# Kernel optimization log

Measured on AMD Instinct MI355X. Metric: run time of the kernel, lower is better.

Reference implementation:

```python
import jax, jax.numpy as jnp
import numpy as np
import math

NFEAT = 1024
NHID = 512
NLAYERS = 8
LAMDA = 0.5
ALPHA = 0.1
N_DIA = 48
DIA_L = 64
N = N_DIA * DIA_L


def setup_inputs() -> dict:
    key = jax.random.key(0)
    ks = jax.random.split(key, 16)
    stdv_fc = 1.0 / math.sqrt(NFEAT)
    stdv_gc = 1.0 / math.sqrt(NHID)
    inp = {
        'a': jax.random.normal(ks[0], (N, NFEAT), jnp.float32),
        'v': jax.random.normal(ks[1], (N, NFEAT), jnp.float32),
        'l': jax.random.normal(ks[2], (N, NFEAT), jnp.float32),
        'W0': jax.random.uniform(ks[3], (NFEAT, NHID), jnp.float32, -stdv_fc, stdv_fc),
        'b0': jax.random.uniform(ks[4], (NHID,), jnp.float32, -stdv_fc, stdv_fc),
        'W1': jax.random.uniform(ks[5], (NFEAT, NHID), jnp.float32, -stdv_fc, stdv_fc),
        'b1': jax.random.uniform(ks[6], (NHID,), jnp.float32, -stdv_fc, stdv_fc),
        'W2': jax.random.uniform(ks[7], (NFEAT, NHID), jnp.float32, -stdv_fc, stdv_fc),
        'b2': jax.random.uniform(ks[8], (NHID,), jnp.float32, -stdv_fc, stdv_fc),
        'Wconv': jax.random.uniform(ks[9], (NLAYERS, NHID, NHID), jnp.float32, -stdv_gc, stdv_gc),
        'dia_len': DIA_L,  # uniform dialogue length
        'topicLabel': jnp.zeros((N,), jnp.int64),
    }
    return inp


def create_big_adj(a, v, l, dia_l):
    n = a.shape[0]
    d = n // dia_l
    feats = jnp.stack([a, v, l])                    # [3, N, F]
    x = feats.reshape(3, d, dia_l, -1)              # [3, D, L, F]
    nrm = x / jnp.sqrt(jnp.sum(x * x, axis=-1, keepdims=True))
    cos = jnp.einsum('mdif,mdjf->mdij', nrm, nrm) * 0.99999
    sim = jnp.arccos(cos)                           # [3, D, L, L]
    adj = jnp.zeros((3 * n, 3 * n), dtype=a.dtype)
    base = jnp.arange(d)[:, None, None] * dia_l     # dialogue start offsets
    rows = jnp.broadcast_to(base + jnp.arange(dia_l)[:, None], (d, dia_l, dia_l))
    cols = jnp.broadcast_to(base + jnp.arange(dia_l)[None, :], (d, dia_l, dia_l))
    for m in range(3):  # same-modality block-diagonal acos-similarity blocks
        adj = adj.at[m * n + rows, m * n + cols].set(sim[m])
    k = jnp.arange(n)
    for m in range(3):  # cross-modal: same-utterance links set to 0.99999
        for mm in range(3):
            if m != mm:
                adj = adj.at[m * n + k, mm * n + k].set(0.99999)
    dsum = jnp.sum(adj, axis=1)
    dinv = dsum ** -0.5
    return dinv[:, None] * adj * dinv[None, :]


def reference(a, v, l, W0, b0, W1, b1, W2, b2, Wconv, dia_len, topicLabel):
    relu = jax.nn.relu
    # eval mode: dropout is identity
    a_ = relu(a @ W0 + b0)
    l_ = relu(l @ W1 + b1)
    v_ = relu(v @ W2 + b2)
    x = jnp.concatenate([a_, v_, l_], axis=0)       # [3N, nhidden]
    adj = create_big_adj(a, v, l, dia_len)
    h0 = x
    h = x
    for i in range(NLAYERS):
        theta = math.log(LAMDA / (i + 1) + 1.0)
        hi = adj @ h
        support = (1.0 - ALPHA) * hi + ALPHA * h0
        h = relu(theta * (support @ Wconv[i]) + (1.0 - theta) * support)
    n = a.shape[0]
    out = jnp.concatenate([h[:n], h[n:2 * n], h[2 * n:]], axis=-1)  # [N, 3*nhidden]
    out = jnp.concatenate([l, out], axis=-1)        # use_residue
    return out
```

## Files before the change

### kernel.cpp

```cpp
#include <hip/hip_runtime.h>
#include <hip/hip_bf16.h>
#include <cmath>

#define NFEAT 1024
#define NHID  512
#define NLAYERS 8
#define NDIA 48
#define DIAL 64
#define NROW (NDIA*DIAL)
#define NROW3 (3*NROW)

typedef short bf16x8 __attribute__((ext_vector_type(8)));
typedef float f32x4  __attribute__((ext_vector_type(4)));
typedef unsigned short u16x8 __attribute__((ext_vector_type(8)));
typedef unsigned short u16x4 __attribute__((ext_vector_type(4)));
typedef unsigned short ushort_t;

__device__ __forceinline__ unsigned short f2bf(float x) {
  __hip_bfloat16 h = __float2bfloat16(x);
  return __builtin_bit_cast(unsigned short, h);
}
__device__ __forceinline__ float bf2f(unsigned short u) {
  __hip_bfloat16 h = __builtin_bit_cast(__hip_bfloat16, u);
  return __bfloat162float(h);
}

__device__ __forceinline__ void gload16(const void* g, void* l) {
  __builtin_amdgcn_global_load_lds(
      (const __attribute__((address_space(1))) void*)g,
      (__attribute__((address_space(3))) void*)l, 16, 0, 0);
}

__global__ __launch_bounds__(256) void k_prep(const float* __restrict__ a, const float* __restrict__ v,
                      const float* __restrict__ l, ushort_t* __restrict__ Abuf,
                      ushort_t* __restrict__ Xn) {
  int gid = blockIdx.x * 256 + threadIdx.x;
  int row = gid >> 6, lane = gid & 63;
  int m = row / NROW, r = row % NROW;
  const float* src = (m == 0 ? a : (m == 1 ? v : l)) + (size_t)r * NFEAT;
  float4 x[4];
  float s = 0.f;
#pragma unroll
  for (int q = 0; q < 4; ++q) {
    x[q] = *reinterpret_cast<const float4*>(src + lane * 4 + q * 256);
    s += x[q].x*x[q].x + x[q].y*x[q].y + x[q].z*x[q].z + x[q].w*x[q].w;
  }
#pragma unroll
  for (int off = 32; off; off >>= 1) s += __shfl_xor(s, off);
  float inv = rsqrtf(s);
  ushort_t* da = Abuf + (size_t)row * NFEAT;
  ushort_t* dn = Xn + (size_t)row * NFEAT;
#pragma unroll
  for (int q = 0; q < 4; ++q) {
    u16x4 oa, on;
    oa[0] = f2bf(x[q].x); oa[1] = f2bf(x[q].y); oa[2] = f2bf(x[q].z); oa[3] = f2bf(x[q].w);
    on[0] = f2bf(x[q].x * inv); on[1] = f2bf(x[q].y * inv);
    on[2] = f2bf(x[q].z * inv); on[3] = f2bf(x[q].w * inv);
    *reinterpret_cast<u16x4*>(da + lane * 4 + q * 256) = oa;
    *reinterpret_cast<u16x4*>(dn + lane * 4 + q * 256) = on;
  }
}

__global__ __launch_bounds__(256) void k_simm(const ushort_t* __restrict__ Xn,
                      ushort_t* __restrict__ Sbf, float* __restrict__ dinv) {
  __shared__ short Xs[2][4096];
  __shared__ float simS[64][73];
  int blk = blockIdx.x;
  const ushort_t* Xb = Xn + (size_t)blk * 64 * NFEAT;
  int t = threadIdx.x, w = t >> 6, lane = t & 63;
  f32x4 acc[4] = {};

#define STAGE_SIM(b, k0) do { \
    _Pragma("unroll") \
    for (int q = 0; q < 2; ++q) { \
      int f_ = t * 8 + q * 2048; \
      int row_ = f_ >> 6; \
      int col_ = (f_ & 63) ^ ((row_ & 7) << 3); \
      gload16(Xb + (size_t)row_ * NFEAT + (k0) + col_, (void*)(Xs[b] + q * 2048 + w * 512)); \
    } } while (0)

  STAGE_SIM(0, 0);
  __syncthreads();
  for (int it = 0; it < 16; ++it) {
    int cur = it & 1;
    if (it < 15) STAGE_SIM(cur ^ 1, (it + 1) * 64);
    const char* base = (const char*)Xs[cur];
#pragma unroll
    for (int ks = 0; ks < 2; ++ks) {
      int koff = ks * 32 + (lane >> 4) * 8;
      int arow = w * 16 + (lane & 15);
      bf16x8 af = *(const bf16x8*)(base + (((arow << 7) + (koff << 1)) ^ ((arow & 7) << 4)));
#pragma unroll
      for (int j = 0; j < 4; ++j) {
        int brow = j * 16 + (lane & 15);
        bf16x8 bf = *(const bf16x8*)(base + (((brow << 7) + (koff << 1)) ^ ((brow & 7) << 4)));
        acc[j] = __builtin_amdgcn_mfma_f32_16x16x32_bf16(af, bf, acc[j], 0, 0, 0);
      }
    }
    __syncthreads();
  }
#undef STAGE_SIM

#pragma unroll
  for (int j = 0; j < 4; ++j)
#pragma unroll
    for (int e = 0; e < 4; ++e) {
      int r = w * 16 + (lane >> 4) * 4 + e;
      int c = j * 16 + (lane & 15);
      float cc = acc[j][e] * 0.99999f;
      cc = fminf(fmaxf(cc, -0.99999f), 0.99999f);
      simS[r][c] = acosf(cc);
    }
  __syncthreads();
  if (t < 64) {
    float s = 0.f;
#pragma unroll 8
    for (int c = 0; c < 64; ++c) s += simS[t][c];
    float di = rsqrtf(s + 1.99998f);
    simS[t][64] = di;
    dinv[blk * 64 + t] = di;
  }
  __syncthreads();
  ushort_t* Sb = Sbf + (size_t)blk * 4096;
#pragma unroll
  for (int q = 0; q < 2; ++q) {
    int idx = t * 8 + q * 2048;
    int i = idx >> 6, j0 = idx & 63;
    float di = simS[i][64];
    u16x8 o;
#pragma unroll
    for (int e = 0; e < 8; ++e)
      o[e] = f2bf(simS[i][j0 + e] * di * simS[j0 + e][64]);
    *reinterpret_cast<u16x8*>(Sb + idx) = o;
  }
}

__global__ void k_cvt_w(const float* __restrict__ s0, const float* __restrict__ s1,
                        const float* __restrict__ s2, ushort_t* __restrict__ dst,
                        int K, int mode) {
  __shared__ float tile[32][33];
  int z = blockIdx.z;
  const float* src = (mode == 1) ? (s0 + (size_t)z * K * NHID)
                                 : (z == 0 ? s0 : (z == 1 ? s1 : s2));
  ushort_t* d = dst + (size_t)z * NHID * K;
  int n0 = blockIdx.x * 32, k0 = blockIdx.y * 32;
  int tx = threadIdx.x & 31, ty = threadIdx.x >> 5;
#pragma unroll
  for (int q = 0; q < 4; ++q)
    tile[ty + q * 8][tx] = src[(size_t)(k0 + ty + q * 8) * NHID + n0 + tx];
  __syncthreads();
#pragma unroll
  for (int q = 0; q < 4; ++q)
    d[(size_t)(n0 + ty + q * 8) * K + k0 + tx] = f2bf(tile[tx][ty + q * 8]);
}

template<int EPI>
__global__ __launch_bounds__(256) void k_gemm_mfma(
    const ushort_t* __restrict__ A, const ushort_t* __restrict__ B,
    const float* __restrict__ ba, const float* __restrict__ bv, const float* __restrict__ bl,
    const ushort_t* __restrict__ sup, ushort_t* __restrict__ C, ushort_t* __restrict__ C2,
    int K, float theta) {
  __shared__ short As[2][128 * 64];
  __shared__ short Bs[2][64 * 64];
  int t = threadIdx.x;
  int w = t >> 6, lane = t & 63;
  int bm = blockIdx.x * 128, bn = blockIdx.y * 64;
  const float* bias = ba;
  if (EPI == 0) {
    int band = bm / NROW;
    B += (size_t)band * NHID * K;
    bias = (band == 0 ? ba : (band == 1 ? bv : bl));
  }
  const ushort_t* Ab = A + (size_t)bm * K;
  const ushort_t* Bb = B + (size_t)bn * K;
  int wr = (w >> 1) * 64, wc = (w & 1) * 32;
  f32x4 acc[4][2] = {};

#define STAGE_G(b, k0) do { \
    _Pragma("unroll") \
    for (int q = 0; q < 4; ++q) { \
      int f_ = t * 8 + q * 2048; int row_ = f_ >> 6; \
      int col_ = (f_ & 63) ^ ((row_ & 7) << 3); \
      gload16(Ab + (size_t)row_ * K + (k0) + col_, (void*)(As[b] + q * 2048 + w * 512)); } \
    _Pragma("unroll") \
    for (int q = 0; q < 2; ++q) { \
      int f_ = t * 8 + q * 2048; int row_ = f_ >> 6; \
      int col_ = (f_ & 63) ^ ((row_ & 7) << 3); \
      gload16(Bb + (size_t)row_ * K + (k0) + col_, (void*)(Bs[b] + q * 2048 + w * 512)); } \
  } while (0)

  STAGE_G(0, 0);
  __syncthreads();
  int T = K >> 6;
  for (int s = 0; s < T; ++s) {
    int cur = s & 1;
    if (s + 1 < T) STAGE_G(cur ^ 1, (s + 1) * 64);
    const char* ab = (const char*)As[cur];
    const char* bb = (const char*)Bs[cur];
#pragma unroll
    for (int ks = 0; ks < 2; ++ks) {
      bf16x8 af[4], bfr[2];
#pragma unroll
      for (int i = 0; i < 4; ++i) {
        int arow = wr + i * 16 + (lane & 15);
        int abo = (arow << 7) + ((ks * 32 + (lane >> 4) * 8) << 1);
        af[i] = *reinterpret_cast<const bf16x8*>(ab + (abo ^ ((arow & 7) << 4)));
      }
#pragma unroll
      for (int j = 0; j < 2; ++j) {
        int brow = wc + j * 16 + (lane & 15);
        int bbo = (brow << 7) + ((ks * 32 + (lane >> 4) * 8) << 1);
        bfr[j] = *reinterpret_cast<const bf16x8*>(bb + (bbo ^ ((brow & 7) << 4)));
      }
#pragma unroll
      for (int i = 0; i < 4; ++i)
#pragma unroll
        for (int j = 0; j < 2; ++j)
          acc[i][j] = __builtin_amdgcn_mfma_f32_16x16x32_bf16(af[i], bfr[j], acc[i][j], 0, 0, 0);
    }
    __syncthreads();
  }
#undef STAGE_G

#pragma unroll
  for (int i = 0; i < 4; ++i) {
#pragma unroll
    for (int jf = 0; jf < 2; ++jf) {
      int r0 = bm + wr + i * 16 + (lane >> 4) * 4;
      int c  = bn + wc + jf * 16 + (lane & 15);
#pragma unroll
      for (int j = 0; j < 4; ++j) {
        int r = r0 + j;
        float val = acc[i][jf][j];
        if (EPI == 0) {
          val = fmaxf(val + bias[c], 0.f);
          unsigned short o = f2bf(val);
          C[(size_t)r * NHID + c] = o;
          C2[(size_t)r * NHID + c] = o;
        } else {
          float s = bf2f(sup[(size_t)r * NHID + c]);
          val = fmaxf(theta * val + (1.f - theta) * s, 0.f);
          C[(size_t)r * NHID + c] = f2bf(val);
        }
      }
    }
  }
}

__global__ __launch_bounds__(256) void k_adj(const ushort_t* __restrict__ Sbf,
                      const ushort_t* __restrict__ h, const ushort_t* __restrict__ h0,
                      const float* __restrict__ dinv, ushort_t* __restrict__ sup) {
  __shared__ short Ss[3 * 4096];
  __shared__ short Ht[3][64][72];
  __shared__ float supS[64][69];
  int d = blockIdx.x, c0 = blockIdx.y * 64;
  int t = threadIdx.x, w = t >> 6, lane = t & 63;
#pragma unroll
  for (int q = 0; q < 6; ++q) {
    int f = t * 8 + q * 2048;
    int mod = f >> 12, rem = f & 4095;
    int row = rem >> 6;
    int col = (rem & 63) ^ ((row & 7) << 3);
    gload16(Sbf + ((size_t)(mod * NDIA + d)) * 4096 + row * 64 + col,
            (void*)(Ss + q * 2048 + w * 512));
  }
#pragma unroll
  for (int q = 0; q < 6; ++q) {
    int idx = t + q * 256;
    int mod = idx >> 9, rem = idx & 511;
    int j = rem >> 3, n0 = (rem & 7) * 8;
    int key = rem & 7;
    u16x8 hv = *reinterpret_cast<const u16x8*>(
        h + ((size_t)(mod * NROW + d * 64 + j)) * NHID + c0 + n0);
    int js = j ^ (key << 3);
#pragma unroll
    for (int e = 0; e < 8; ++e) Ht[mod][n0 + e][js] = hv[e];
  }
  __syncthreads();
  f32x4 acc[3][4] = {};
#pragma unroll
  for (int m = 0; m < 3; ++m)
#pragma unroll
    for (int ks = 0; ks < 2; ++ks) {
      int koff = ks * 32 + (lane >> 4) * 8;
      int arow = w * 16 + (lane & 15);
      bf16x8 af = *(const bf16x8*)((const char*)Ss + m * 8192 +
                    (((arow << 7) + (koff << 1)) ^ ((arow & 7) << 4)));
#pragma unroll
      for (int j = 0; j < 4; ++j) {
        int n = j * 16 + (lane & 15);
        int koff_s = koff ^ (((n >> 3) & 7) << 3);
        bf16x8 bf = *(const bf16x8*)(&Ht[m][n][koff_s]);
        acc[m][j] = __builtin_amdgcn_mfma_f32_16x16x32_bf16(af, bf, acc[m][j], 0, 0, 0);
      }
    }
  int r = t >> 2, cc0 = (t & 3) * 16;
  int u = d * 64 + r;
  float d0 = dinv[u], d1 = dinv[NROW + u], d2 = dinv[2 * NROW + u];
  float dv[3] = {d0, d1, d2};
  for (int m = 0; m < 3; ++m) {
#pragma unroll
    for (int j = 0; j < 4; ++j)
#pragma unroll
      for (int e = 0; e < 4; ++e)
        supS[w * 16 + (lane >> 4) * 4 + e][j * 16 + (lane & 15)] = acc[m][j][e];
    __syncthreads();
    int mm1 = (m + 1) % 3, mm2 = (m + 2) % 3;
    int g = m * NROW + u;
    float c1 = 0.99999f * dv[m] * dv[mm1];
    float c2 = 0.99999f * dv[m] * dv[mm2];
    const ushort_t* p1 = h + ((size_t)(mm1 * NROW + u)) * NHID + c0 + cc0;
    const ushort_t* p2 = h + ((size_t)(mm2 * NROW + u)) * NHID + c0 + cc0;
    const ushort_t* pz = h0 + (size_t)g * NHID + c0 + cc0;
    ushort_t* po = sup + (size_t)g * NHID + c0 + cc0;
#pragma unroll
    for (int half = 0; half < 2; ++half) {
      u16x8 h1 = *reinterpret_cast<const u16x8*>(p1 + half * 8);
      u16x8 h2 = *reinterpret_cast<const u16x8*>(p2 + half * 8);
      u16x8 hz = *reinterpret_cast<const u16x8*>(pz + half * 8);
      u16x8 o;
#pragma unroll
      for (int e = 0; e < 8; ++e) {
        float val = 0.9f * (supS[r][cc0 + half * 8 + e] + c1 * bf2f(h1[e]) + c2 * bf2f(h2[e]))
                  + 0.1f * bf2f(hz[e]);
        o[e] = f2bf(val);
      }
      *reinterpret_cast<u16x8*>(po + half * 8) = o;
    }
    __syncthreads();
  }
}

__global__ void k_out(const float* __restrict__ l, const ushort_t* __restrict__ h,
                      float* __restrict__ out) {
  int idx = blockIdx.x * blockDim.x + threadIdx.x;
  int i = idx / 640;
  int c4 = (idx % 640) * 4;
  float4 val;
  if (c4 < 1024) {
    val = *reinterpret_cast<const float4*>(l + (size_t)i * NFEAT + c4);
  } else {
    int cc = c4 - 1024;
    int m = cc >> 9, c = cc & 511;
    u16x4 hv = *reinterpret_cast<const u16x4*>(h + ((size_t)m * NROW + i) * NHID + c);
    val.x = bf2f(hv[0]); val.y = bf2f(hv[1]); val.z = bf2f(hv[2]); val.w = bf2f(hv[3]);
  }
  *reinterpret_cast<float4*>(out + (size_t)i * 2560 + c4) = val;
}

extern "C" void kernel_launch(void* const* d_in, const int* in_sizes, int n_in,
                              void* d_out, int out_size, void* d_ws, size_t ws_size,
                              hipStream_t stream) {
  const float* a  = (const float*)d_in[0];
  const float* v  = (const float*)d_in[1];
  const float* l  = (const float*)d_in[2];
  const float* W0 = (const float*)d_in[3];
  const float* b0 = (const float*)d_in[4];
  const float* W1 = (const float*)d_in[5];
  const float* b1 = (const float*)d_in[6];
  const float* W2 = (const float*)d_in[7];
  const float* b2 = (const float*)d_in[8];
  const float* Wc = (const float*)d_in[9];
  float* out = (float*)d_out;

  const size_t SZ = (size_t)NROW3 * NHID;
  const size_t XSZ = (size_t)3 * NROW * NFEAT;
  char* ws = (char*)d_ws;
  ushort_t* Abuf = (ushort_t*)ws;  ws += XSZ * 2;
  ushort_t* Xn   = (ushort_t*)ws;  ws += XSZ * 2;
  ushort_t* h0   = (ushort_t*)ws;  ws += SZ * 2;
  ushort_t* Wtfc = (ushort_t*)ws;  ws += (size_t)3 * NHID * NFEAT * 2;
  ushort_t* Wct  = (ushort_t*)ws;  ws += (size_t)NLAYERS * NHID * NHID * 2;
  ushort_t* Sbf  = (ushort_t*)ws;  ws += (size_t)144 * 4096 * 2;
  float* dinv    = (float*)ws;
  ushort_t* h   = Xn;
  ushort_t* sup = Xn + SZ;

  k_prep<<<NROW3 / 4, 256, 0, stream>>>(a, v, l, Abuf, Xn);
  k_cvt_w<<<dim3(NHID / 32, NFEAT / 32, 3), 256, 0, stream>>>(W0, W2, W1, Wtfc, NFEAT, 0);
  k_cvt_w<<<dim3(NHID / 32, NHID / 32, NLAYERS), 256, 0, stream>>>(Wc, nullptr, nullptr, Wct, NHID, 1);
  k_simm<<<3 * NDIA, 256, 0, stream>>>(Xn, Sbf, dinv);

  k_gemm_mfma<0><<<dim3(NROW3 / 128, NHID / 64), 256, 0, stream>>>(
      Abuf, Wtfc, b0, b2, b1, nullptr, h0, h, NFEAT, 0.f);

  for (int i = 0; i < NLAYERS; ++i) {
    float theta = (float)std::log(0.5 / (i + 1) + 1.0);
    k_adj<<<dim3(NDIA, NHID / 64), 256, 0, stream>>>(Sbf, h, h0, dinv, sup);
    k_gemm_mfma<1><<<dim3(NROW3 / 128, NHID / 64), 256, 0, stream>>>(
        sup, Wct + (size_t)i * NHID * NHID, nullptr, nullptr, nullptr, sup, h, nullptr, NHID, theta);
  }

  k_out<<<(NROW * 2560 / 4) / 256, 256, 0, stream>>>(l, h, out);
}
```

Baseline: 235.0 us.

## Remap block order for XCD locality and reuse staged support tile in epilogue

The GEMM and adjacency kernels now use a 1D grid whose linear block index is remapped so that blocks sharing the same row band (or dialogue) land on the same XCD, which should improve L2 reuse across the eight-way round-robin dispatch. In the layer GEMM epilogue, the support residual values are now read from the A tile already staged in LDS at the K-step that matches the block's column range, instead of being reloaded from global memory. This removes a redundant global read per output element, at the cost of extra registers for the cached values and an assumption that K equals NHID.

```diff
diff --git a/kernel.cpp b/kernel.cpp
--- a/kernel.cpp
+++ b/kernel.cpp
@@ -158,13 +158,16 @@
 __global__ __launch_bounds__(256) void k_gemm_mfma(
     const ushort_t* __restrict__ A, const ushort_t* __restrict__ B,
     const float* __restrict__ ba, const float* __restrict__ bv, const float* __restrict__ bl,
-    const ushort_t* __restrict__ sup, ushort_t* __restrict__ C, ushort_t* __restrict__ C2,
+    ushort_t* __restrict__ C, ushort_t* __restrict__ C2,
     int K, float theta) {
   __shared__ short As[2][128 * 64];
   __shared__ short Bs[2][64 * 64];
   int t = threadIdx.x;
   int w = t >> 6, lane = t & 63;
-  int bm = blockIdx.x * 128, bn = blockIdx.y * 64;
+  int lin = blockIdx.x;
+  int logical = (lin & 7) * 72 + (lin >> 3);
+  int bx = logical >> 3, by = logical & 7;
+  int bm = bx * 128, bn = by * 64;
   const float* bias = ba;
   if (EPI == 0) {
     int band = bm / NROW;
@@ -175,6 +178,8 @@
   const ushort_t* Bb = B + (size_t)bn * K;
   int wr = (w >> 1) * 64, wc = (w & 1) * 32;
   f32x4 acc[4][2] = {};
+  float supr[4][2][4];
+  int sup_step = bn >> 6;
 
 #define STAGE_G(b, k0) do { \
     _Pragma("unroll") \
@@ -197,6 +202,19 @@
     if (s + 1 < T) STAGE_G(cur ^ 1, (s + 1) * 64);
     const char* ab = (const char*)As[cur];
     const char* bb = (const char*)Bs[cur];
+    if (EPI == 1 && s == sup_step) {
+#pragma unroll
+      for (int i = 0; i < 4; ++i)
+#pragma unroll
+        for (int jf = 0; jf < 2; ++jf)
+#pragma unroll
+          for (int j = 0; j < 4; ++j) {
+            int ar = wr + i * 16 + (lane >> 4) * 4 + j;
+            int gc = wc + jf * 16 + (lane & 15);
+            supr[i][jf][j] = bf2f(*(const ushort_t*)(
+                ab + ((ar << 7) + ((gc << 1) ^ ((ar & 7) << 4)))));
+          }
+    }
 #pragma unroll
     for (int ks = 0; ks < 2; ++ks) {
       bf16x8 af[4], bfr[2];
@@ -238,8 +256,7 @@
           C[(size_t)r * NHID + c] = o;
           C2[(size_t)r * NHID + c] = o;
         } else {
-          float s = bf2f(sup[(size_t)r * NHID + c]);
-          val = fmaxf(theta * val + (1.f - theta) * s, 0.f);
+          val = fmaxf(theta * val + (1.f - theta) * supr[i][jf][j], 0.f);
           C[(size_t)r * NHID + c] = f2bf(val);
         }
       }
@@ -253,7 +270,9 @@
   __shared__ short Ss[3 * 4096];
   __shared__ short Ht[3][64][72];
   __shared__ float supS[64][69];
-  int d = blockIdx.x, c0 = blockIdx.y * 64;
+  int lin = blockIdx.x;
+  int logical = (lin & 7) * 48 + (lin >> 3);
+  int d = logical >> 3, c0 = (logical & 7) * 64;
   int t = threadIdx.x, w = t >> 6, lane = t & 63;
 #pragma unroll
   for (int q = 0; q < 6; ++q) {
@@ -381,14 +400,13 @@
   k_cvt_w<<<dim3(NHID / 32, NHID / 32, NLAYERS), 256, 0, stream>>>(Wc, nullptr, nullptr, Wct, NHID, 1);
   k_simm<<<3 * NDIA, 256, 0, stream>>>(Xn, Sbf, dinv);
 
-  k_gemm_mfma<0><<<dim3(NROW3 / 128, NHID / 64), 256, 0, stream>>>(
-      Abuf, Wtfc, b0, b2, b1, nullptr, h0, h, NFEAT, 0.f);
+  k_gemm_mfma<0><<<576, 256, 0, stream>>>(Abuf, Wtfc, b0, b2, b1, h0, h, NFEAT, 0.f);
 
   for (int i = 0; i < NLAYERS; ++i) {
     float theta = (float)std::log(0.5 / (i + 1) + 1.0);
-    k_adj<<<dim3(NDIA, NHID / 64), 256, 0, stream>>>(Sbf, h, h0, dinv, sup);
-    k_gemm_mfma<1><<<dim3(NROW3 / 128, NHID / 64), 256, 0, stream>>>(
-        sup, Wct + (size_t)i * NHID * NHID, nullptr, nullptr, nullptr, sup, h, nullptr, NHID, theta);
+    k_adj<<<384, 256, 0, stream>>>(Sbf, h, h0, dinv, sup);
+    k_gemm_mfma<1><<<576, 256, 0, stream>>>(
+        sup, Wct + (size_t)i * NHID * NHID, nullptr, nullptr, nullptr, h, nullptr, NHID, theta);
   }
 
   k_out<<<(NROW * 2560 / 4) / 256, 256, 0, stream>>>(l, h, out);
```

Result: slower. 247.8 us (+5.5%).

## Fuse adjacency propagation and layer GEMM into one per-layer kernel

Applied to the files above, without the earlier changes.

Replaces the per-layer pair of kernels (adjacency aggregation writing `sup` to global memory, then the MFMA GEMM reading it back) with a single kernel. Each block handles one dialogue, one modality and half of the output columns. It computes the 64-row support tile over all 512 hidden columns into LDS, then multiplies it by the layer weight and writes h to a ping-pong buffer. This removes the global round trip for the support tensor and halves the launches per layer. The cost is ~157KB of LDS per block, only 288 blocks, and the adjacency product recomputed twice per tile, once for each column half.

```diff
diff --git a/kernel.cpp b/kernel.cpp
--- a/kernel.cpp
+++ b/kernel.cpp
@@ -154,23 +154,19 @@
     d[(size_t)(n0 + ty + q * 8) * K + k0 + tx] = f2bf(tile[tx][ty + q * 8]);
 }
 
-template<int EPI>
-__global__ __launch_bounds__(256) void k_gemm_mfma(
+__global__ __launch_bounds__(256) void k_fc(
     const ushort_t* __restrict__ A, const ushort_t* __restrict__ B,
     const float* __restrict__ ba, const float* __restrict__ bv, const float* __restrict__ bl,
-    const ushort_t* __restrict__ sup, ushort_t* __restrict__ C, ushort_t* __restrict__ C2,
-    int K, float theta) {
+    ushort_t* __restrict__ C, ushort_t* __restrict__ C2) {
   __shared__ short As[2][128 * 64];
   __shared__ short Bs[2][64 * 64];
+  const int K = NFEAT;
   int t = threadIdx.x;
   int w = t >> 6, lane = t & 63;
   int bm = blockIdx.x * 128, bn = blockIdx.y * 64;
-  const float* bias = ba;
-  if (EPI == 0) {
-    int band = bm / NROW;
-    B += (size_t)band * NHID * K;
-    bias = (band == 0 ? ba : (band == 1 ? bv : bl));
-  }
+  int band = bm / NROW;
+  B += (size_t)band * NHID * K;
+  const float* bias = (band == 0 ? ba : (band == 1 ? bv : bl));
   const ushort_t* Ab = A + (size_t)bm * K;
   const ushort_t* Bb = B + (size_t)bn * K;
   int wr = (w >> 1) * 64, wc = (w & 1) * 32;
@@ -191,7 +187,7 @@
 
   STAGE_G(0, 0);
   __syncthreads();
-  int T = K >> 6;
+  const int T = K >> 6;
   for (int s = 0; s < T; ++s) {
     int cur = s & 1;
     if (s + 1 < T) STAGE_G(cur ^ 1, (s + 1) * 64);
@@ -231,103 +227,172 @@
 #pragma unroll
       for (int j = 0; j < 4; ++j) {
         int r = r0 + j;
-        float val = acc[i][jf][j];
-        if (EPI == 0) {
-          val = fmaxf(val + bias[c], 0.f);
-          unsigned short o = f2bf(val);
-          C[(size_t)r * NHID + c] = o;
-          C2[(size_t)r * NHID + c] = o;
-        } else {
-          float s = bf2f(sup[(size_t)r * NHID + c]);
-          val = fmaxf(theta * val + (1.f - theta) * s, 0.f);
-          C[(size_t)r * NHID + c] = f2bf(val);
-        }
-      }
-    }
-  }
-}
-
-__global__ __launch_bounds__(256) void k_adj(const ushort_t* __restrict__ Sbf,
-                      const ushort_t* __restrict__ h, const ushort_t* __restrict__ h0,
-                      const float* __restrict__ dinv, ushort_t* __restrict__ sup) {
-  __shared__ short Ss[3 * 4096];
-  __shared__ short Ht[3][64][72];
-  __shared__ float supS[64][69];
-  int d = blockIdx.x, c0 = blockIdx.y * 64;
+        float val = fmaxf(acc[i][jf][j] + bias[c], 0.f);
+        unsigned short o = f2bf(val);
+        C[(size_t)r * NHID + c] = o;
+        C2[(size_t)r * NHID + c] = o;
+      }
+    }
+  }
+}
+
+__global__ __launch_bounds__(256) void k_layer(
+    const ushort_t* __restrict__ Sbf, const ushort_t* __restrict__ Wct_i,
+    const ushort_t* __restrict__ hin, const ushort_t* __restrict__ h0,
+    const float* __restrict__ dinv, ushort_t* __restrict__ hout, float theta) {
+  __shared__ char lds[160768];
+  ushort_t* supL   = (ushort_t*)lds;
+  short* Ss        = (short*)(lds + 65536);
+  short (*Ht)[68]  = (short (*)[68])(lds + 73728);
+  float (*supS)[68]= (float (*)[68])(lds + 143360);
+  short* Bs        = (short*)(lds + 65536);
+
+  int lin = blockIdx.x;
+  int d = lin / 6, rem = lin % 6;
+  int m = rem >> 1, half = rem & 1;
+  int bn = half * 256;
   int t = threadIdx.x, w = t >> 6, lane = t & 63;
-#pragma unroll
-  for (int q = 0; q < 6; ++q) {
+  int m1 = (m == 2) ? 0 : m + 1, m2 = (m == 0) ? 2 : m - 1;
+  int g0 = m * NROW + d * 64, g1 = m1 * NROW + d * 64, g2 = m2 * NROW + d * 64;
+
+  const ushort_t* Sb = Sbf + (size_t)(m * NDIA + d) * 4096;
+#pragma unroll
+  for (int q = 0; q < 2; ++q) {
     int f = t * 8 + q * 2048;
-    int mod = f >> 12, rem = f & 4095;
-    int row = rem >> 6;
-    int col = (rem & 63) ^ ((row & 7) << 3);
-    gload16(Sbf + ((size_t)(mod * NDIA + d)) * 4096 + row * 64 + col,
-            (void*)(Ss + q * 2048 + w * 512));
-  }
-#pragma unroll
-  for (int q = 0; q < 6; ++q) {
-    int idx = t + q * 256;
-    int mod = idx >> 9, rem = idx & 511;
-    int j = rem >> 3, n0 = (rem & 7) * 8;
-    int key = rem & 7;
-    u16x8 hv = *reinterpret_cast<const u16x8*>(
-        h + ((size_t)(mod * NROW + d * 64 + j)) * NHID + c0 + n0);
-    int js = j ^ (key << 3);
-#pragma unroll
-    for (int e = 0; e < 8; ++e) Ht[mod][n0 + e][js] = hv[e];
-  }
-  __syncthreads();
-  f32x4 acc[3][4] = {};
-#pragma unroll
-  for (int m = 0; m < 3; ++m)
+    int row = f >> 6, col = (f & 63) ^ ((row & 7) << 3);
+    gload16(Sb + row * 64 + col, (void*)(Ss + q * 2048 + w * 512));
+  }
+#pragma unroll
+  for (int q = 0; q < 16; ++q) {
+    int j = w + q * 4;
+    int n0 = (t & 63) * 8;
+    u16x8 hv = *reinterpret_cast<const u16x8*>(hin + (size_t)(g0 + j) * NHID + n0);
+    int js = j ^ ((t & 7) << 3);
+#pragma unroll
+    for (int e = 0; e < 8; ++e) Ht[n0 + e][js] = hv[e];
+  }
+
+  int rr = t >> 2, c16 = (t & 3) * 16;
+  int u = d * 64 + rr;
+  float dm = dinv[m * NROW + u];
+  float c1 = 0.99999f * dm * dinv[m1 * NROW + u];
+  float c2 = 0.99999f * dm * dinv[m2 * NROW + u];
+
+  u16x8 pf[2][6];
+#define PF(slot, kc) do { \
+    const ushort_t* q1 = hin + (size_t)(g1 + rr) * NHID + (kc) * 64 + c16; \
+    const ushort_t* q2 = hin + (size_t)(g2 + rr) * NHID + (kc) * 64 + c16; \
+    const ushort_t* qz = h0 + (size_t)(g0 + rr) * NHID + (kc) * 64 + c16;  \
+    pf[slot][0] = *(const u16x8*)q1; pf[slot][1] = *(const u16x8*)(q1 + 8); \
+    pf[slot][2] = *(const u16x8*)q2; pf[slot][3] = *(const u16x8*)(q2 + 8); \
+    pf[slot][4] = *(const u16x8*)qz; pf[slot][5] = *(const u16x8*)(qz + 8); \
+  } while (0)
+  PF(0, 0);
+  __syncthreads();
+
+  f32x4 accc[8][4] = {};
+  int arow = w * 16 + (lane & 15);
+#pragma unroll
+  for (int ks = 0; ks < 2; ++ks) {
+    int koff = ks * 32 + (lane >> 4) * 8;
+    bf16x8 af = *(const bf16x8*)((const char*)Ss +
+                  (((arow << 7) + (koff << 1)) ^ ((arow & 7) << 4)));
+#pragma unroll
+    for (int kc = 0; kc < 8; ++kc)
+#pragma unroll
+      for (int j = 0; j < 4; ++j) {
+        int n = kc * 64 + j * 16 + (lane & 15);
+        int koff_s = koff ^ (((n >> 3) & 7) << 3);
+        bf16x8 bf = *(const bf16x8*)(&Ht[n][koff_s]);
+        accc[kc][j] = __builtin_amdgcn_mfma_f32_16x16x32_bf16(af, bf, accc[kc][j], 0, 0, 0);
+      }
+  }
+
+#pragma unroll
+  for (int kc = 0; kc < 8; ++kc) {
+    if (kc < 7) PF((kc + 1) & 1, kc + 1);
+#pragma unroll
+    for (int j = 0; j < 4; ++j)
+#pragma unroll
+      for (int e = 0; e < 4; ++e)
+        supS[w * 16 + (lane >> 4) * 4 + e][j * 16 + (lane & 15)] = accc[kc][j][e];
+    __syncthreads();
+    const u16x8* P = pf[kc & 1];
+#pragma unroll
+    for (int hh = 0; hh < 2; ++hh) {
+      u16x8 o;
+#pragma unroll
+      for (int e = 0; e < 8; ++e) {
+        float val = 0.9f * (supS[rr][c16 + hh * 8 + e]
+                    + c1 * bf2f(P[hh][e]) + c2 * bf2f(P[2 + hh][e]))
+                  + 0.1f * bf2f(P[4 + hh][e]);
+        o[e] = f2bf(val);
+      }
+      int byte = rr * 1024 + (kc * 64 + c16 + hh * 8) * 2;
+      *reinterpret_cast<u16x8*>((char*)supL + (byte ^ ((rr & 7) << 4))) = o;
+    }
+    __syncthreads();
+  }
+#undef PF
+
+  const ushort_t* Wb = Wct_i + (size_t)bn * NHID;
+#define STAGE_W(b, k0) do { \
+    _Pragma("unroll") \
+    for (int q = 0; q < 8; ++q) { \
+      int f = t * 8 + q * 2048; \
+      int n_ = f >> 6, col = (f & 63) ^ ((n_ & 7) << 3); \
+      gload16(Wb + (size_t)n_ * NHID + (k0) + col, (void*)(Bs + (b) * 16384 + q * 2048 + w * 512)); \
+    } } while (0)
+
+  f32x4 acc[4][4] = {};
+  STAGE_W(0, 0);
+  __syncthreads();
+#pragma unroll 1
+  for (int s = 0; s < 8; ++s) {
+    int cur = s & 1;
+    if (s < 7) STAGE_W(cur ^ 1, (s + 1) * 64);
+    const char* bb = (const char*)(Bs + cur * 16384);
 #pragma unroll
     for (int ks = 0; ks < 2; ++ks) {
       int koff = ks * 32 + (lane >> 4) * 8;
-      int arow = w * 16 + (lane & 15);
-      bf16x8 af = *(const bf16x8*)((const char*)Ss + m * 8192 +
-                    (((arow << 7) + (koff << 1)) ^ ((arow & 7) << 4)));
+      bf16x8 af[4], bfr[4];
+#pragma unroll
+      for (int i = 0; i < 4; ++i) {
+        int ar = i * 16 + (lane & 15);
+        af[i] = *(const bf16x8*)((const char*)supL +
+                 ((ar * 1024 + (s * 64 + koff) * 2) ^ ((ar & 7) << 4)));
+      }
 #pragma unroll
       for (int j = 0; j < 4; ++j) {
-        int n = j * 16 + (lane & 15);
-        int koff_s = koff ^ (((n >> 3) & 7) << 3);
-        bf16x8 bf = *(const bf16x8*)(&Ht[m][n][koff_s]);
-        acc[m][j] = __builtin_amdgcn_mfma_f32_16x16x32_bf16(af, bf, acc[m][j], 0, 0, 0);
-      }
-    }
-  int r = t >> 2, cc0 = (t & 3) * 16;
-  int u = d * 64 + r;
-  float d0 = dinv[u], d1 = dinv[NROW + u], d2 = dinv[2 * NROW + u];
-  float dv[3] = {d0, d1, d2};
-  for (int m = 0; m < 3; ++m) {
-#pragma unroll
-    for (int j = 0; j < 4; ++j)
-#pragma unroll
-      for (int e = 0; e < 4; ++e)
-        supS[w * 16 + (lane >> 4) * 4 + e][j * 16 + (lane & 15)] = acc[m][j][e];
+        int nl = w * 64 + j * 16 + (lane & 15);
+        bfr[j] = *(const bf16x8*)(bb + (((nl << 7) + (koff << 1)) ^ ((nl & 7) << 4)));
+      }
+#pragma unroll
+      for (int i = 0; i < 4; ++i)
+#pragma unroll
+        for (int j = 0; j < 4; ++j)
+          acc[i][j] = __builtin_amdgcn_mfma_f32_16x16x32_bf16(af[i], bfr[j], acc[i][j], 0, 0, 0);
+    }
     __syncthreads();
-    int mm1 = (m + 1) % 3, mm2 = (m + 2) % 3;
-    int g = m * NROW + u;
-    float c1 = 0.99999f * dv[m] * dv[mm1];
-    float c2 = 0.99999f * dv[m] * dv[mm2];
-    const ushort_t* p1 = h + ((size_t)(mm1 * NROW + u)) * NHID + c0 + cc0;
-    const ushort_t* p2 = h + ((size_t)(mm2 * NROW + u)) * NHID + c0 + cc0;
-    const ushort_t* pz = h0 + (size_t)g * NHID + c0 + cc0;
-    ushort_t* po = sup + (size_t)g * NHID + c0 + cc0;
-#pragma unroll
-    for (int half = 0; half < 2; ++half) {
-      u16x8 h1 = *reinterpret_cast<const u16x8*>(p1 + half * 8);
-      u16x8 h2 = *reinterpret_cast<const u16x8*>(p2 + half * 8);
-      u16x8 hz = *reinterpret_cast<const u16x8*>(pz + half * 8);
-      u16x8 o;
-#pragma unroll
-      for (int e = 0; e < 8; ++e) {
-        float val = 0.9f * (supS[r][cc0 + half * 8 + e] + c1 * bf2f(h1[e]) + c2 * bf2f(h2[e]))
-                  + 0.1f * bf2f(hz[e]);
-        o[e] = f2bf(val);
-      }
-      *reinterpret_cast<u16x8*>(po + half * 8) = o;
-    }
-    __syncthreads();
+  }
+#undef STAGE_W
+
+  float omt = 1.f - theta;
+#pragma unroll
+  for (int i = 0; i < 4; ++i) {
+#pragma unroll
+    for (int j = 0; j < 4; ++j) {
+      int cl = w * 64 + j * 16 + (lane & 15);
+      int cg = bn + cl;
+#pragma unroll
+      for (int e = 0; e < 4; ++e) {
+        int r = i * 16 + (lane >> 4) * 4 + e;
+        float supv = bf2f(*(const ushort_t*)((const char*)supL +
+                       ((r * 1024 + cg * 2) ^ ((r & 7) << 4))));
+        float val = fmaxf(theta * acc[i][j][e] + omt * supv, 0.f);
+        hout[(size_t)(g0 + r) * NHID + cg] = f2bf(val);
+      }
+    }
   }
 }
 
@@ -373,23 +438,24 @@
   ushort_t* Wct  = (ushort_t*)ws;  ws += (size_t)NLAYERS * NHID * NHID * 2;
   ushort_t* Sbf  = (ushort_t*)ws;  ws += (size_t)144 * 4096 * 2;
   float* dinv    = (float*)ws;
-  ushort_t* h   = Xn;
-  ushort_t* sup = Xn + SZ;
+  ushort_t* hA = Xn;
+  ushort_t* hB = Xn + SZ;
 
   k_prep<<<NROW3 / 4, 256, 0, stream>>>(a, v, l, Abuf, Xn);
   k_cvt_w<<<dim3(NHID / 32, NFEAT / 32, 3), 256, 0, stream>>>(W0, W2, W1, Wtfc, NFEAT, 0);
   k_cvt_w<<<dim3(NHID / 32, NHID / 32, NLAYERS), 256, 0, stream>>>(Wc, nullptr, nullptr, Wct, NHID, 1);
   k_simm<<<3 * NDIA, 256, 0, stream>>>(Xn, Sbf, dinv);
 
-  k_gemm_mfma<0><<<dim3(NROW3 / 128, NHID / 64), 256, 0, stream>>>(
-      Abuf, Wtfc, b0, b2, b1, nullptr, h0, h, NFEAT, 0.f);
-
+  k_fc<<<dim3(NROW3 / 128, NHID / 64), 256, 0, stream>>>(Abuf, Wtfc, b0, b2, b1, h0, hA);
+
+  ushort_t* cur = hA;
+  ushort_t* nxt = hB;
   for (int i = 0; i < NLAYERS; ++i) {
     float theta = (float)std::log(0.5 / (i + 1) + 1.0);
-    k_adj<<<dim3(NDIA, NHID / 64), 256, 0, stream>>>(Sbf, h, h0, dinv, sup);
-    k_gemm_mfma<1><<<dim3(NROW3 / 128, NHID / 64), 256, 0, stream>>>(
-        sup, Wct + (size_t)i * NHID * NHID, nullptr, nullptr, nullptr, sup, h, nullptr, NHID, theta);
-  }
-
-  k_out<<<(NROW * 2560 / 4) / 256, 256, 0, stream>>>(l, h, out);
-}
+    k_layer<<<288, 256, 0, stream>>>(Sbf, Wct + (size_t)i * NHID * NHID,
+                                     cur, h0, dinv, nxt, theta);
+    ushort_t* tmp = cur; cur = nxt; nxt = tmp;
+  }
+
+  k_out<<<(NROW * 2560 / 4) / 256, 256, 0, stream>>>(l, cur, out);
+}
```

New measurement: 433.5 us. 84.5% more time.

## Fuse GCNII layer loop into persistent kernel with grid-wide atomic barriers

Applied to the files above, without the earlier changes.

Replaces the 16 per-layer kernel launches (adjacency aggregation plus dense GEMM) with one persistent 384-block kernel. It alternates the two phases and separates them with a software grid barrier built from an atomic counter and a spin-wait. The layer GEMM is also retiled to 96x128 so it uses the same 384-block grid, with shared memory reused between phases. This aims to remove launch gaps and tail effects between small kernels. It relies on all 384 blocks being co-resident, two per CU, which is checked with an occupancy query, and falls back to separate launches otherwise. The spin barrier has a timeout cap and adds fence and atomic overhead per phase.

```diff
diff --git a/kernel.cpp b/kernel.cpp
--- a/kernel.cpp
+++ b/kernel.cpp
@@ -16,6 +16,8 @@
 typedef unsigned short u16x4 __attribute__((ext_vector_type(4)));
 typedef unsigned short ushort_t;
 
+struct Thetas { float th[NLAYERS]; };
+
 __device__ __forceinline__ unsigned short f2bf(float x) {
   __hip_bfloat16 h = __float2bfloat16(x);
   return __builtin_bit_cast(unsigned short, h);
@@ -29,6 +31,20 @@
   __builtin_amdgcn_global_load_lds(
       (const __attribute__((address_space(1))) void*)g,
       (__attribute__((address_space(3))) void*)l, 16, 0, 0);
+}
+
+__device__ __forceinline__ void gbar(unsigned* bar, unsigned target) {
+  __threadfence();
+  __syncthreads();
+  if (threadIdx.x == 0) {
+    __hip_atomic_fetch_add(bar, 1u, __ATOMIC_RELEASE, __HIP_MEMORY_SCOPE_AGENT);
+    int cap = 50000000;
+    while (__hip_atomic_load(bar, __ATOMIC_ACQUIRE, __HIP_MEMORY_SCOPE_AGENT) < target) {
+      __builtin_amdgcn_s_sleep(2);
+      if (--cap == 0) break;
+    }
+  }
+  __syncthreads();
 }
 
 __global__ __launch_bounds__(256) void k_prep(const float* __restrict__ a, const float* __restrict__ v,
@@ -154,23 +170,19 @@
     d[(size_t)(n0 + ty + q * 8) * K + k0 + tx] = f2bf(tile[tx][ty + q * 8]);
 }
 
-template<int EPI>
-__global__ __launch_bounds__(256) void k_gemm_mfma(
+__global__ __launch_bounds__(256) void k_fc(
     const ushort_t* __restrict__ A, const ushort_t* __restrict__ B,
     const float* __restrict__ ba, const float* __restrict__ bv, const float* __restrict__ bl,
-    const ushort_t* __restrict__ sup, ushort_t* __restrict__ C, ushort_t* __restrict__ C2,
-    int K, float theta) {
+    ushort_t* __restrict__ C, ushort_t* __restrict__ C2) {
   __shared__ short As[2][128 * 64];
   __shared__ short Bs[2][64 * 64];
+  const int K = NFEAT;
   int t = threadIdx.x;
   int w = t >> 6, lane = t & 63;
   int bm = blockIdx.x * 128, bn = blockIdx.y * 64;
-  const float* bias = ba;
-  if (EPI == 0) {
-    int band = bm / NROW;
-    B += (size_t)band * NHID * K;
-    bias = (band == 0 ? ba : (band == 1 ? bv : bl));
-  }
+  int band = bm / NROW;
+  B += (size_t)band * NHID * K;
+  const float* bias = (band == 0 ? ba : (band == 1 ? bv : bl));
   const ushort_t* Ab = A + (size_t)bm * K;
   const ushort_t* Bb = B + (size_t)bn * K;
   int wr = (w >> 1) * 64, wc = (w & 1) * 32;
@@ -191,7 +203,7 @@
 
   STAGE_G(0, 0);
   __syncthreads();
-  int T = K >> 6;
+  const int T = K >> 6;
   for (int s = 0; s < T; ++s) {
     int cur = s & 1;
     if (s + 1 < T) STAGE_G(cur ^ 1, (s + 1) * 64);
@@ -231,30 +243,23 @@
 #pragma unroll
       for (int j = 0; j < 4; ++j) {
         int r = r0 + j;
-        float val = acc[i][jf][j];
-        if (EPI == 0) {
-          val = fmaxf(val + bias[c], 0.f);
-          unsigned short o = f2bf(val);
-          C[(size_t)r * NHID + c] = o;
-          C2[(size_t)r * NHID + c] = o;
-        } else {
-          float s = bf2f(sup[(size_t)r * NHID + c]);
-          val = fmaxf(theta * val + (1.f - theta) * s, 0.f);
-          C[(size_t)r * NHID + c] = f2bf(val);
-        }
-      }
-    }
-  }
-}
-
-__global__ __launch_bounds__(256) void k_adj(const ushort_t* __restrict__ Sbf,
-                      const ushort_t* __restrict__ h, const ushort_t* __restrict__ h0,
-                      const float* __restrict__ dinv, ushort_t* __restrict__ sup) {
-  __shared__ short Ss[3 * 4096];
-  __shared__ short Ht[3][64][72];
-  __shared__ float supS[64][69];
-  int d = blockIdx.x, c0 = blockIdx.y * 64;
+        float val = fmaxf(acc[i][jf][j] + bias[c], 0.f);
+        unsigned short o = f2bf(val);
+        C[(size_t)r * NHID + c] = o;
+        C2[(size_t)r * NHID + c] = o;
+      }
+    }
+  }
+}
+
+__device__ __forceinline__ void phaseA_dev(int b, const ushort_t* __restrict__ Sbf,
+    const ushort_t* __restrict__ h, const ushort_t* __restrict__ h0,
+    const float* __restrict__ dinv, ushort_t* __restrict__ sup, char* lds) {
+  short* Ss = (short*)lds;
+  short (*Ht)[72] = (short (*)[72])(lds + 24576);
+  float (*supS)[69] = (float (*)[69])lds;
   int t = threadIdx.x, w = t >> 6, lane = t & 63;
+  int d = b >> 3, c0 = (b & 7) << 6;
 #pragma unroll
   for (int q = 0; q < 6; ++q) {
     int f = t * 8 + q * 2048;
@@ -274,7 +279,7 @@
         h + ((size_t)(mod * NROW + d * 64 + j)) * NHID + c0 + n0);
     int js = j ^ (key << 3);
 #pragma unroll
-    for (int e = 0; e < 8; ++e) Ht[mod][n0 + e][js] = hv[e];
+    for (int e = 0; e < 8; ++e) Ht[mod * 64 + n0 + e][js] = hv[e];
   }
   __syncthreads();
   f32x4 acc[3][4] = {};
@@ -290,14 +295,14 @@
       for (int j = 0; j < 4; ++j) {
         int n = j * 16 + (lane & 15);
         int koff_s = koff ^ (((n >> 3) & 7) << 3);
-        bf16x8 bf = *(const bf16x8*)(&Ht[m][n][koff_s]);
+        bf16x8 bf = *(const bf16x8*)(&Ht[m * 64 + n][koff_s]);
         acc[m][j] = __builtin_amdgcn_mfma_f32_16x16x32_bf16(af, bf, acc[m][j], 0, 0, 0);
       }
     }
+  __syncthreads();
   int r = t >> 2, cc0 = (t & 3) * 16;
   int u = d * 64 + r;
-  float d0 = dinv[u], d1 = dinv[NROW + u], d2 = dinv[2 * NROW + u];
-  float dv[3] = {d0, d1, d2};
+  float dv[3] = {dinv[u], dinv[NROW + u], dinv[2 * NROW + u]};
   for (int m = 0; m < 3; ++m) {
 #pragma unroll
     for (int j = 0; j < 4; ++j)
@@ -329,6 +334,110 @@
     }
     __syncthreads();
   }
+}
+
+__device__ __forceinline__ void phaseB_dev(int b, const ushort_t* __restrict__ sup,
+    const ushort_t* __restrict__ Wl, ushort_t* __restrict__ h, float theta, char* lds) {
+  short* As0 = (short*)lds;
+  short* Bs0 = (short*)(lds + 24576);
+  int t = threadIdx.x, w = t >> 6, lane = t & 63;
+  int bm = (b >> 2) * 96, bn = (b & 3) * 128;
+  const ushort_t* Ab = sup + (size_t)bm * NHID;
+  const ushort_t* Bb = Wl + (size_t)bn * NHID;
+  f32x4 acc[6][2] = {};
+
+#define STAGE_B(bb_, k0) do { \
+    _Pragma("unroll") \
+    for (int q = 0; q < 3; ++q) { \
+      int f_ = t * 8 + q * 2048; int row_ = f_ >> 6; \
+      int col_ = (f_ & 63) ^ ((row_ & 7) << 3); \
+      gload16(Ab + (size_t)row_ * NHID + (k0) + col_, (void*)(As0 + (bb_) * 6144 + q * 2048 + w * 512)); } \
+    _Pragma("unroll") \
+    for (int q = 0; q < 4; ++q) { \
+      int f_ = t * 8 + q * 2048; int row_ = f_ >> 6; \
+      int col_ = (f_ & 63) ^ ((row_ & 7) << 3); \
+      gload16(Bb + (size_t)row_ * NHID + (k0) + col_, (void*)(Bs0 + (bb_) * 8192 + q * 2048 + w * 512)); } \
+  } while (0)
+
+  STAGE_B(0, 0);
+  __syncthreads();
+  for (int s = 0; s < 8; ++s) {
+    int cur = s & 1;
+    if (s + 1 < 8) STAGE_B(cur ^ 1, (s + 1) * 64);
+    const char* ab = (const char*)(As0 + cur * 6144);
+    const char* bb = (const char*)(Bs0 + cur * 8192);
+#pragma unroll
+    for (int ks = 0; ks < 2; ++ks) {
+      int koff = ks * 32 + (lane >> 4) * 8;
+      bf16x8 af[6], bfr[2];
+#pragma unroll
+      for (int i = 0; i < 6; ++i) {
+        int arow = i * 16 + (lane & 15);
+        af[i] = *reinterpret_cast<const bf16x8*>(ab +
+                  (((arow << 7) + (koff << 1)) ^ ((arow & 7) << 4)));
+      }
+#pragma unroll
+      for (int j = 0; j < 2; ++j) {
+        int brow = w * 32 + j * 16 + (lane & 15);
+        bfr[j] = *reinterpret_cast<const bf16x8*>(bb +
+                  (((brow << 7) + (koff << 1)) ^ ((brow & 7) << 4)));
+      }
+#pragma unroll
+      for (int i = 0; i < 6; ++i)
+#pragma unroll
+        for (int j = 0; j < 2; ++j)
+          acc[i][j] = __builtin_amdgcn_mfma_f32_16x16x32_bf16(af[i], bfr[j], acc[i][j], 0, 0, 0);
+    }
+    __syncthreads();
+  }
+#undef STAGE_B
+
+  float omt = 1.f - theta;
+#pragma unroll
+  for (int i = 0; i < 6; ++i) {
+#pragma unroll
+    for (int j = 0; j < 2; ++j) {
+      int c = bn + w * 32 + j * 16 + (lane & 15);
+      int r0 = bm + i * 16 + (lane >> 4) * 4;
+#pragma unroll
+      for (int e = 0; e < 4; ++e) {
+        int r = r0 + e;
+        float sv = bf2f(sup[(size_t)r * NHID + c]);
+        float val = fmaxf(theta * acc[i][j][e] + omt * sv, 0.f);
+        h[(size_t)r * NHID + c] = f2bf(val);
+      }
+    }
+  }
+}
+
+__global__ __launch_bounds__(256, 2) void k_sync(
+    const ushort_t* __restrict__ Sbf, const ushort_t* __restrict__ Wct,
+    ushort_t* __restrict__ h, ushort_t* __restrict__ sup,
+    const ushort_t* __restrict__ h0, const float* __restrict__ dinv,
+    unsigned* bar, Thetas Th) {
+  __shared__ char lds[57344];
+  int b = blockIdx.x;
+  unsigned target = 0;
+  for (int L = 0; L < NLAYERS; ++L) {
+    phaseA_dev(b, Sbf, h, h0, dinv, sup, lds);
+    target += 384; gbar(bar, target);
+    phaseB_dev(b, sup, Wct + (size_t)L * NHID * NHID, h, Th.th[L], lds);
+    target += 384; gbar(bar, target);
+  }
+}
+
+__global__ __launch_bounds__(256, 2) void k_adj1(
+    const ushort_t* __restrict__ Sbf, const ushort_t* __restrict__ h,
+    const ushort_t* __restrict__ h0, const float* __restrict__ dinv,
+    ushort_t* __restrict__ sup) {
+  __shared__ char lds[52224];
+  phaseA_dev(blockIdx.x, Sbf, h, h0, dinv, sup, lds);
+}
+__global__ __launch_bounds__(256, 2) void k_gemm1(
+    const ushort_t* __restrict__ sup, const ushort_t* __restrict__ Wl,
+    ushort_t* __restrict__ h, float theta) {
+  __shared__ char lds[57344];
+  phaseB_dev(blockIdx.x, sup, Wl, h, theta, lds);
 }
 
 __global__ void k_out(const float* __restrict__ l, const ushort_t* __restrict__ h,
@@ -372,23 +481,34 @@
   ushort_t* Wtfc = (ushort_t*)ws;  ws += (size_t)3 * NHID * NFEAT * 2;
   ushort_t* Wct  = (ushort_t*)ws;  ws += (size_t)NLAYERS * NHID * NHID * 2;
   ushort_t* Sbf  = (ushort_t*)ws;  ws += (size_t)144 * 4096 * 2;
-  float* dinv    = (float*)ws;
+  float* dinv    = (float*)ws;     ws += (size_t)NROW3 * 4;
+  unsigned* bar  = (unsigned*)ws;
   ushort_t* h   = Xn;
   ushort_t* sup = Xn + SZ;
+
+  hipMemsetAsync(bar, 0, 256, stream);
 
   k_prep<<<NROW3 / 4, 256, 0, stream>>>(a, v, l, Abuf, Xn);
   k_cvt_w<<<dim3(NHID / 32, NFEAT / 32, 3), 256, 0, stream>>>(W0, W2, W1, Wtfc, NFEAT, 0);
   k_cvt_w<<<dim3(NHID / 32, NHID / 32, NLAYERS), 256, 0, stream>>>(Wc, nullptr, nullptr, Wct, NHID, 1);
   k_simm<<<3 * NDIA, 256, 0, stream>>>(Xn, Sbf, dinv);
 
-  k_gemm_mfma<0><<<dim3(NROW3 / 128, NHID / 64), 256, 0, stream>>>(
-      Abuf, Wtfc, b0, b2, b1, nullptr, h0, h, NFEAT, 0.f);
-
-  for (int i = 0; i < NLAYERS; ++i) {
-    float theta = (float)std::log(0.5 / (i + 1) + 1.0);
-    k_adj<<<dim3(NDIA, NHID / 64), 256, 0, stream>>>(Sbf, h, h0, dinv, sup);
-    k_gemm_mfma<1><<<dim3(NROW3 / 128, NHID / 64), 256, 0, stream>>>(
-        sup, Wct + (size_t)i * NHID * NHID, nullptr, nullptr, nullptr, sup, h, nullptr, NHID, theta);
+  k_fc<<<dim3(NROW3 / 128, NHID / 64), 256, 0, stream>>>(Abuf, Wtfc, b0, b2, b1, h0, h);
+
+  Thetas Th;
+  for (int i = 0; i < NLAYERS; ++i)
+    Th.th[i] = (float)std::log(0.5 / (i + 1) + 1.0);
+
+  int maxb = 0;
+  hipError_t oerr = hipOccupancyMaxActiveBlocksPerMultiprocessor(
+      &maxb, reinterpret_cast<const void*>(k_sync), 256, 0);
+  if (oerr == hipSuccess && maxb >= 2) {
+    k_sync<<<384, 256, 0, stream>>>(Sbf, Wct, h, sup, h0, dinv, bar, Th);
+  } else {
+    for (int i = 0; i < NLAYERS; ++i) {
+      k_adj1<<<384, 256, 0, stream>>>(Sbf, h, h0, dinv, sup);
+      k_gemm1<<<384, 256, 0, stream>>>(sup, Wct + (size_t)i * NHID * NHID, h, Th.th[i]);
+    }
   }
 
   k_out<<<(NROW * 2560 / 4) / 256, 256, 0, stream>>>(l, h, out);
```

Result: no change. 239.3 us (+1.8%).
